# Performance work log

Measured on AMD Instinct MI355X. Metric: run time of the kernel, lower is better.

The kernel has to match this reference:

```python
import jax, jax.numpy as jnp
import numpy as np


def setup_inputs() -> dict:
    key = jax.random.key(0)
    k1, k2 = jax.random.split(key)
    B, C, D = 131072, 1024, 512
    x = jax.random.normal(k1, (B, D), dtype=jnp.float32)
    centers = jax.random.normal(k2, (C, D), dtype=jnp.float32)
    return {"x": x, "centers": centers}


def reference(x, centers):
    x_sq = jnp.sum(x * x, axis=1, keepdims=True)            # [B, 1]
    c_sq = jnp.sum(centers * centers, axis=1)               # [C]
    cross = jnp.einsum('bd,cd->bc', x, centers)             # [B, C]
    distances = jnp.maximum(x_sq + c_sq[None, :] - 2.0 * cross, 0.0)
    # softmin over clusters = softmax(-distances)
    prob = jax.nn.softmax(-distances, axis=1)
    return (distances, prob)
```

## Files before the change

kernel.cpp:

```cpp
#include <hip/hip_runtime.h>
#include <stdint.h>

#define NROWS 131072
#define NC 1024
#define ND 512
#define BM 32

using f32x4   = __attribute__((ext_vector_type(4))) float;
using bf16x8  = __attribute__((ext_vector_type(8))) short;
using short2v = __attribute__((ext_vector_type(2))) short;
using float2v = __attribute__((ext_vector_type(2))) float;
using float4v = __attribute__((ext_vector_type(4))) float;

__device__ __forceinline__ uint16_t f32_bf16(float f) {
  uint32_t u = __builtin_bit_cast(uint32_t, f);
  u += 0x7FFFu + ((u >> 16) & 1u);
  return (uint16_t)(u >> 16);
}
__device__ __forceinline__ float bf16_f32(uint16_t h) {
  uint32_t u = ((uint32_t)h) << 16;
  return __builtin_bit_cast(float, u);
}

__device__ __forceinline__ void gload_lds16(const void* g, void* l) {
  __builtin_amdgcn_global_load_lds(
      (const __attribute__((address_space(1))) unsigned int*)g,
      (__attribute__((address_space(3))) unsigned int*)l, 16, 0, 0);
}

__global__ __launch_bounds__(64) void prep_centers(
    const float* __restrict__ centers,
    uint16_t* __restrict__ cs_hi, uint16_t* __restrict__ cs_lo,
    float* __restrict__ csq) {
  const int c = blockIdx.x;
  const int t = threadIdx.x;
  const float* row = centers + (size_t)c * ND;
  const int k0 = t * 8;
  float v[8];
#pragma unroll
  for (int i = 0; i < 8; ++i) v[i] = row[k0 + i];
  float ss = 0.f;
#pragma unroll
  for (int i = 0; i < 8; ++i) ss += v[i] * v[i];
#pragma unroll
  for (int m = 1; m < 64; m <<= 1) ss += __shfl_xor(ss, m);
  if (t == 0) csq[c] = ss;

  const int kk = t >> 2;
  const int j  = t & 3;
  const int p  = j ^ (c & 3);
  const size_t off = (size_t)kk * 32768 + (size_t)c * 32 + (size_t)p * 8;
#pragma unroll
  for (int i = 0; i < 8; ++i) {
    uint16_t h = f32_bf16(v[i]);
    uint16_t l = f32_bf16(v[i] - bf16_f32(h));
    cs_hi[off + i] = h;
    cs_lo[off + i] = l;
  }
}

__global__ __launch_bounds__(512)
__attribute__((amdgpu_waves_per_eu(4)))
void kmeans_fused(
    const float* __restrict__ x,
    const uint16_t* __restrict__ cs_hi, const uint16_t* __restrict__ cs_lo,
    const float* __restrict__ csq,
    float* __restrict__ dist, float* __restrict__ prob) {
  __shared__ __align__(16) char bs[65536];
  __shared__ __align__(16) char as_hi[2048];
  __shared__ __align__(16) char as_lo[2048];
  __shared__ float xsq[BM];

  const int tid  = threadIdx.x;
  const int lane = tid & 63;
  const int wid  = tid >> 6;
  const int row0 = blockIdx.x * BM;
  const int ar = tid >> 4;
  const int ac = tid & 15;

  auto stage = [&](const uint16_t* base, int kk) {
    const char* srcb = (const char*)(base + (size_t)kk * 32768);
#pragma unroll
    for (int i = 0; i < 8; ++i) {
      const int o = (tid + i * 512) * 16;
      gload_lds16(srcb + o, bs + o);
    }
  };
  auto xload = [&](int kk) -> float2v {
    return *(const float2v*)(x + (size_t)(row0 + ar) * ND + kk * 32 + ac * 2);
  };
  auto awrite = [&](float2v v) {
    const int p = (ac >> 2) ^ (ar & 3);
    const int off = ar * 64 + p * 16 + (ac & 3) * 4;
    short2v h, l;
#pragma unroll
    for (int i = 0; i < 2; ++i) {
      uint16_t hb = f32_bf16(v[i]);
      h[i] = (short)hb;
      l[i] = (short)f32_bf16(v[i] - bf16_f32(hb));
    }
    *(short2v*)(as_hi + off) = h;
    *(short2v*)(as_lo + off) = l;
  };

  f32x4 acc[2][8];
  const f32x4 z = {0.f, 0.f, 0.f, 0.f};
#pragma unroll
  for (int mr = 0; mr < 2; ++mr)
#pragma unroll
    for (int n = 0; n < 8; ++n) acc[mr][n] = z;

  const int swz  = (((lane >> 4) ^ (lane & 3)) << 4);
  const int aoff = (lane & 15) * 64 + swz;
  const int boff = (wid * 128 + (lane & 15)) * 64 + swz;

  float xacc = 0.f;

#pragma unroll 1
  for (int s = 0; s < 16; ++s) {
    stage(cs_hi, s);
    float2v v = xload(s);
    awrite(v);
    xacc += v[0] * v[0] + v[1] * v[1];
    __syncthreads();
    {
      bf16x8 ah0 = *(const bf16x8*)(as_hi + aoff);
      bf16x8 ah1 = *(const bf16x8*)(as_hi + aoff + 1024);
      bf16x8 al0 = *(const bf16x8*)(as_lo + aoff);
      bf16x8 al1 = *(const bf16x8*)(as_lo + aoff + 1024);
#pragma unroll
      for (int n = 0; n < 8; ++n) {
        bf16x8 b = *(const bf16x8*)(bs + boff + n * 1024);
        acc[0][n] = __builtin_amdgcn_mfma_f32_16x16x32_bf16(ah0, b, acc[0][n], 0, 0, 0);
        acc[1][n] = __builtin_amdgcn_mfma_f32_16x16x32_bf16(ah1, b, acc[1][n], 0, 0, 0);
        acc[0][n] = __builtin_amdgcn_mfma_f32_16x16x32_bf16(al0, b, acc[0][n], 0, 0, 0);
        acc[1][n] = __builtin_amdgcn_mfma_f32_16x16x32_bf16(al1, b, acc[1][n], 0, 0, 0);
      }
    }
    __syncthreads();
  }

#pragma unroll 1
  for (int s = 0; s < 16; ++s) {
    stage(cs_lo, s);
    float2v v = xload(s);
    awrite(v);
    __syncthreads();
    {
      bf16x8 ah0 = *(const bf16x8*)(as_hi + aoff);
      bf16x8 ah1 = *(const bf16x8*)(as_hi + aoff + 1024);
#pragma unroll
      for (int n = 0; n < 8; ++n) {
        bf16x8 b = *(const bf16x8*)(bs + boff + n * 1024);
        acc[0][n] = __builtin_amdgcn_mfma_f32_16x16x32_bf16(ah0, b, acc[0][n], 0, 0, 0);
        acc[1][n] = __builtin_amdgcn_mfma_f32_16x16x32_bf16(ah1, b, acc[1][n], 0, 0, 0);
      }
    }
    __syncthreads();
  }

  xacc += __shfl_xor(xacc, 1);
  xacc += __shfl_xor(xacc, 2);
  xacc += __shfl_xor(xacc, 4);
  xacc += __shfl_xor(xacc, 8);
  if (ac == 0) xsq[ar] = xacc;

  float* ldsT = (float*)bs;
  const int rsub = (lane >> 4) * 4;
#pragma unroll
  for (int p = 0; p < 2; ++p) {
#pragma unroll
    for (int n = 0; n < 8; ++n)
#pragma unroll
      for (int r = 0; r < 4; ++r) {
        const int lrow = rsub + r;
        const int col = wid * 128 + n * 16 + (lane & 15);
        ldsT[lrow * 1024 + (col ^ (((lrow >> 2) & 3) << 3))] = acc[p][n][r];
      }
    __syncthreads();
#pragma unroll
    for (int q = 0; q < 2; ++q) {
      const int lr = wid * 2 + q;
      const size_t grow = (size_t)(row0 + p * 16 + lr);
      const int cmask = ((lr >> 2) & 3) << 3;
      const float xq = xsq[p * 16 + lr];
      float4v dd[4];
      float dmin = 1e30f;
#pragma unroll
      for (int j = 0; j < 4; ++j) {
        const int f = lane * 4 + j * 256;
        float4v raw = *(const float4v*)&ldsT[lr * 1024 + (f ^ cmask)];
        float4v cq = *(const float4v*)(csq + f);
#pragma unroll
        for (int i = 0; i < 4; ++i) {
          float d = fmaxf(xq + cq[i] - 2.0f * raw[i], 0.0f);
          dd[j][i] = d;
          dmin = fminf(dmin, d);
        }
      }
#pragma unroll
      for (int m = 1; m < 64; m <<= 1) dmin = fminf(dmin, __shfl_xor(dmin, m));
#pragma unroll
      for (int j = 0; j < 4; ++j)
        *(float4v*)(dist + grow * NC + lane * 4 + j * 256) = dd[j];
      float ssum = 0.f;
#pragma unroll
      for (int j = 0; j < 4; ++j)
#pragma unroll
        for (int i = 0; i < 4; ++i) {
          float e = __expf(dmin - dd[j][i]);
          dd[j][i] = e;
          ssum += e;
        }
#pragma unroll
      for (int m = 1; m < 64; m <<= 1) ssum += __shfl_xor(ssum, m);
      const float sinv = 1.0f / ssum;
#pragma unroll
      for (int j = 0; j < 4; ++j) {
        float4v pv;
#pragma unroll
        for (int i = 0; i < 4; ++i) pv[i] = dd[j][i] * sinv;
        *(float4v*)(prob + grow * NC + lane * 4 + j * 256) = pv;
      }
    }
    __syncthreads();
  }
}

extern "C" void kernel_launch(void* const* d_in, const int* in_sizes, int n_in,
                              void* d_out, int out_size, void* d_ws, size_t ws_size,
                              hipStream_t stream) {
  const float* x = (const float*)d_in[0];
  const float* centers = (const float*)d_in[1];
  float* dist = (float*)d_out;
  float* prob = dist + (size_t)NROWS * NC;

  uint16_t* cs_hi = (uint16_t*)d_ws;
  uint16_t* cs_lo = cs_hi + (size_t)NC * ND;
  float* csq = (float*)(cs_lo + (size_t)NC * ND);

  prep_centers<<<dim3(NC), dim3(64), 0, stream>>>(centers, cs_hi, cs_lo, csq);
  kmeans_fused<<<dim3(NROWS / BM), dim3(512), 0, stream>>>(x, cs_hi, cs_lo, csq,
                                                           dist, prob);
}
```

Baseline: 717.6 us.

## Double-buffer LDS staging and double the row tile to 64 rows

Raises the block tile from 32 to 64 rows, so each staged center tile feeds four MFMA row groups instead of two, halving center reloads per row. The two K loops merge into one 32-step loop with double-buffered LDS for both center and x tiles, so the next tile's global loads run during the current MFMAs and one barrier per step is removed. The LDS swizzle is changed to match the new x write pattern. Occupancy drops (waves_per_eu 2, about 140KB LDS per block) and accumulator registers double, which could limit latency hiding.

```diff
diff --git a/kernel.cpp b/kernel.cpp
--- a/kernel.cpp
+++ b/kernel.cpp
@@ -4,12 +4,12 @@
 #define NROWS 131072
 #define NC 1024
 #define ND 512
-#define BM 32
+#define BM 64
+#define NSTEP 32
 
 using f32x4   = __attribute__((ext_vector_type(4))) float;
 using bf16x8  = __attribute__((ext_vector_type(8))) short;
-using short2v = __attribute__((ext_vector_type(2))) short;
-using float2v = __attribute__((ext_vector_type(2))) float;
+using short4v = __attribute__((ext_vector_type(4))) short;
 using float4v = __attribute__((ext_vector_type(4))) float;
 
 __device__ __forceinline__ uint16_t f32_bf16(float f) {
@@ -48,7 +48,7 @@
 
   const int kk = t >> 2;
   const int j  = t & 3;
-  const int p  = j ^ (c & 3);
+  const int p  = j ^ ((c >> 1) & 3);
   const size_t off = (size_t)kk * 32768 + (size_t)c * 32 + (size_t)p * 8;
 #pragma unroll
   for (int i = 0; i < 8; ++i) {
@@ -60,101 +60,118 @@
 }
 
 __global__ __launch_bounds__(512)
-__attribute__((amdgpu_waves_per_eu(4)))
+__attribute__((amdgpu_waves_per_eu(2)))
 void kmeans_fused(
     const float* __restrict__ x,
     const uint16_t* __restrict__ cs_hi, const uint16_t* __restrict__ cs_lo,
     const float* __restrict__ csq,
     float* __restrict__ dist, float* __restrict__ prob) {
-  __shared__ __align__(16) char bs[65536];
-  __shared__ __align__(16) char as_hi[2048];
-  __shared__ __align__(16) char as_lo[2048];
+  __shared__ __align__(16) char bs[2][65536];
+  __shared__ __align__(16) char as_hi[2][4096];
+  __shared__ __align__(16) char as_lo[2][4096];
   __shared__ float xsq[BM];
 
   const int tid  = threadIdx.x;
   const int lane = tid & 63;
   const int wid  = tid >> 6;
   const int row0 = blockIdx.x * BM;
-  const int ar = tid >> 4;
-  const int ac = tid & 15;
-
-  auto stage = [&](const uint16_t* base, int kk) {
-    const char* srcb = (const char*)(base + (size_t)kk * 32768);
+  const int ar = tid >> 3;
+  const int ac = tid & 7;
+
+  auto stage = [&](int s) {
+    const uint16_t* base = (s < 16) ? cs_hi : cs_lo;
+    const char* srcb = (const char*)(base + (size_t)(s & 15) * 32768);
+    char* dst = bs[s & 1];
 #pragma unroll
     for (int i = 0; i < 8; ++i) {
       const int o = (tid + i * 512) * 16;
-      gload_lds16(srcb + o, bs + o);
-    }
-  };
-  auto xload = [&](int kk) -> float2v {
-    return *(const float2v*)(x + (size_t)(row0 + ar) * ND + kk * 32 + ac * 2);
-  };
-  auto awrite = [&](float2v v) {
-    const int p = (ac >> 2) ^ (ar & 3);
-    const int off = ar * 64 + p * 16 + (ac & 3) * 4;
-    short2v h, l;
-#pragma unroll
-    for (int i = 0; i < 2; ++i) {
+      gload_lds16(srcb + o, dst + o);
+    }
+  };
+  auto xload = [&](int s) -> float4v {
+    return *(const float4v*)(x + (size_t)(row0 + ar) * ND + (s & 15) * 32 + ac * 4);
+  };
+  auto awrite = [&](int s, float4v v) {
+    const int j = ac >> 1;
+    const int p = j ^ ((ar >> 1) & 3);
+    const int off = ar * 64 + p * 16 + (ac & 1) * 8;
+    short4v h, l;
+#pragma unroll
+    for (int i = 0; i < 4; ++i) {
       uint16_t hb = f32_bf16(v[i]);
       h[i] = (short)hb;
       l[i] = (short)f32_bf16(v[i] - bf16_f32(hb));
     }
-    *(short2v*)(as_hi + off) = h;
-    *(short2v*)(as_lo + off) = l;
-  };
-
-  f32x4 acc[2][8];
+    *(short4v*)(as_hi[s & 1] + off) = h;
+    *(short4v*)(as_lo[s & 1] + off) = l;
+  };
+
+  f32x4 acc[4][8];
   const f32x4 z = {0.f, 0.f, 0.f, 0.f};
 #pragma unroll
-  for (int mr = 0; mr < 2; ++mr)
+  for (int mr = 0; mr < 4; ++mr)
 #pragma unroll
     for (int n = 0; n < 8; ++n) acc[mr][n] = z;
 
-  const int swz  = (((lane >> 4) ^ (lane & 3)) << 4);
+  const int swz  = (((lane >> 4) ^ (((lane & 15) >> 1) & 3)) << 4);
   const int aoff = (lane & 15) * 64 + swz;
   const int boff = (wid * 128 + (lane & 15)) * 64 + swz;
 
+  auto compute = [&](int s) {
+    const char* bp  = bs[s & 1];
+    const char* ahp = as_hi[s & 1];
+    bf16x8 ah[4];
+#pragma unroll
+    for (int mr = 0; mr < 4; ++mr)
+      ah[mr] = *(const bf16x8*)(ahp + aoff + mr * 1024);
+    if (s < 16) {
+      const char* alp = as_lo[s & 1];
+      bf16x8 al[4];
+#pragma unroll
+      for (int mr = 0; mr < 4; ++mr)
+        al[mr] = *(const bf16x8*)(alp + aoff + mr * 1024);
+#pragma unroll
+      for (int n = 0; n < 8; ++n) {
+        bf16x8 b = *(const bf16x8*)(bp + boff + n * 1024);
+#pragma unroll
+        for (int mr = 0; mr < 4; ++mr)
+          acc[mr][n] = __builtin_amdgcn_mfma_f32_16x16x32_bf16(ah[mr], b, acc[mr][n], 0, 0, 0);
+#pragma unroll
+        for (int mr = 0; mr < 4; ++mr)
+          acc[mr][n] = __builtin_amdgcn_mfma_f32_16x16x32_bf16(al[mr], b, acc[mr][n], 0, 0, 0);
+      }
+    } else {
+#pragma unroll
+      for (int n = 0; n < 8; ++n) {
+        bf16x8 b = *(const bf16x8*)(bp + boff + n * 1024);
+#pragma unroll
+        for (int mr = 0; mr < 4; ++mr)
+          acc[mr][n] = __builtin_amdgcn_mfma_f32_16x16x32_bf16(ah[mr], b, acc[mr][n], 0, 0, 0);
+      }
+    }
+  };
+
   float xacc = 0.f;
 
+  stage(0);
+  {
+    float4v v0 = xload(0);
+    xacc += v0[0] * v0[0] + v0[1] * v0[1] + v0[2] * v0[2] + v0[3] * v0[3];
+    awrite(0, v0);
+  }
+  __syncthreads();
+
 #pragma unroll 1
-  for (int s = 0; s < 16; ++s) {
-    stage(cs_hi, s);
-    float2v v = xload(s);
-    awrite(v);
-    xacc += v[0] * v[0] + v[1] * v[1];
-    __syncthreads();
-    {
-      bf16x8 ah0 = *(const bf16x8*)(as_hi + aoff);
-      bf16x8 ah1 = *(const bf16x8*)(as_hi + aoff + 1024);
-      bf16x8 al0 = *(const bf16x8*)(as_lo + aoff);
-      bf16x8 al1 = *(const bf16x8*)(as_lo + aoff + 1024);
-#pragma unroll
-      for (int n = 0; n < 8; ++n) {
-        bf16x8 b = *(const bf16x8*)(bs + boff + n * 1024);
-        acc[0][n] = __builtin_amdgcn_mfma_f32_16x16x32_bf16(ah0, b, acc[0][n], 0, 0, 0);
-        acc[1][n] = __builtin_amdgcn_mfma_f32_16x16x32_bf16(ah1, b, acc[1][n], 0, 0, 0);
-        acc[0][n] = __builtin_amdgcn_mfma_f32_16x16x32_bf16(al0, b, acc[0][n], 0, 0, 0);
-        acc[1][n] = __builtin_amdgcn_mfma_f32_16x16x32_bf16(al1, b, acc[1][n], 0, 0, 0);
-      }
-    }
-    __syncthreads();
-  }
-
-#pragma unroll 1
-  for (int s = 0; s < 16; ++s) {
-    stage(cs_lo, s);
-    float2v v = xload(s);
-    awrite(v);
-    __syncthreads();
-    {
-      bf16x8 ah0 = *(const bf16x8*)(as_hi + aoff);
-      bf16x8 ah1 = *(const bf16x8*)(as_hi + aoff + 1024);
-#pragma unroll
-      for (int n = 0; n < 8; ++n) {
-        bf16x8 b = *(const bf16x8*)(bs + boff + n * 1024);
-        acc[0][n] = __builtin_amdgcn_mfma_f32_16x16x32_bf16(ah0, b, acc[0][n], 0, 0, 0);
-        acc[1][n] = __builtin_amdgcn_mfma_f32_16x16x32_bf16(ah1, b, acc[1][n], 0, 0, 0);
-      }
+  for (int s = 0; s < NSTEP; ++s) {
+    if (s + 1 < NSTEP) {
+      float4v vn = xload(s + 1);
+      stage(s + 1);
+      if (s + 1 < 16)
+        xacc += vn[0] * vn[0] + vn[1] * vn[1] + vn[2] * vn[2] + vn[3] * vn[3];
+      compute(s);
+      awrite(s + 1, vn);
+    } else {
+      compute(s);
     }
     __syncthreads();
   }
@@ -162,13 +179,12 @@
   xacc += __shfl_xor(xacc, 1);
   xacc += __shfl_xor(xacc, 2);
   xacc += __shfl_xor(xacc, 4);
-  xacc += __shfl_xor(xacc, 8);
   if (ac == 0) xsq[ar] = xacc;
 
   float* ldsT = (float*)bs;
   const int rsub = (lane >> 4) * 4;
 #pragma unroll
-  for (int p = 0; p < 2; ++p) {
+  for (int p = 0; p < 4; ++p) {
 #pragma unroll
     for (int n = 0; n < 8; ++n)
 #pragma unroll
```

Result: slower. 2.137 ms (+197.9%).

## Double-buffer center tiles and load x fragments directly into registers

Applied to the files above, without the earlier changes.

Replaces the single LDS buffer for center tiles with a double buffer, prefetching the next step's tile and x values while the current step computes. Manual vmcnt waits and raw barriers replace __syncthreads. Each wave now loads its own x fragment straight into registers and converts it to bf16 hi/lo, which removes the LDS staging of A and its per-step barrier. It also changes the B swizzle pattern, raises MFMA priority, and drops the waves_per_eu hint. In exchange it uses 128KB of LDS (limiting occupancy to one block per CU) and has every wave redundantly load and convert x.

```diff
diff --git a/kernel.cpp b/kernel.cpp
--- a/kernel.cpp
+++ b/kernel.cpp
@@ -5,12 +5,14 @@
 #define NC 1024
 #define ND 512
 #define BM 32
+#define NSTEP 32
 
 using f32x4   = __attribute__((ext_vector_type(4))) float;
 using bf16x8  = __attribute__((ext_vector_type(8))) short;
-using short2v = __attribute__((ext_vector_type(2))) short;
-using float2v = __attribute__((ext_vector_type(2))) float;
 using float4v = __attribute__((ext_vector_type(4))) float;
+
+#define WAITV12() asm volatile("s_waitcnt vmcnt(12)" ::: "memory")
+#define WAITV0()  asm volatile("s_waitcnt vmcnt(0)" ::: "memory")
 
 __device__ __forceinline__ uint16_t f32_bf16(float f) {
   uint32_t u = __builtin_bit_cast(uint32_t, f);
@@ -48,7 +50,7 @@
 
   const int kk = t >> 2;
   const int j  = t & 3;
-  const int p  = j ^ (c & 3);
+  const int p  = j ^ ((c >> 1) & 3);
   const size_t off = (size_t)kk * 32768 + (size_t)c * 32 + (size_t)p * 8;
 #pragma unroll
   for (int i = 0; i < 8; ++i) {
@@ -59,48 +61,32 @@
   }
 }
 
-__global__ __launch_bounds__(512)
-__attribute__((amdgpu_waves_per_eu(4)))
-void kmeans_fused(
+__global__ __launch_bounds__(512) void kmeans_fused(
     const float* __restrict__ x,
     const uint16_t* __restrict__ cs_hi, const uint16_t* __restrict__ cs_lo,
     const float* __restrict__ csq,
     float* __restrict__ dist, float* __restrict__ prob) {
-  __shared__ __align__(16) char bs[65536];
-  __shared__ __align__(16) char as_hi[2048];
-  __shared__ __align__(16) char as_lo[2048];
+  __shared__ __align__(16) char bs[2][65536];
   __shared__ float xsq[BM];
 
   const int tid  = threadIdx.x;
   const int lane = tid & 63;
   const int wid  = tid >> 6;
   const int row0 = blockIdx.x * BM;
-  const int ar = tid >> 4;
-  const int ac = tid & 15;
-
-  auto stage = [&](const uint16_t* base, int kk) {
-    const char* srcb = (const char*)(base + (size_t)kk * 32768);
-#pragma unroll
-    for (int i = 0; i < 8; ++i) {
-      const int o = (tid + i * 512) * 16;
-      gload_lds16(srcb + o, bs + o);
-    }
-  };
-  auto xload = [&](int kk) -> float2v {
-    return *(const float2v*)(x + (size_t)(row0 + ar) * ND + kk * 32 + ac * 2);
-  };
-  auto awrite = [&](float2v v) {
-    const int p = (ac >> 2) ^ (ar & 3);
-    const int off = ar * 64 + p * 16 + (ac & 3) * 4;
-    short2v h, l;
-#pragma unroll
-    for (int i = 0; i < 2; ++i) {
-      uint16_t hb = f32_bf16(v[i]);
-      h[i] = (short)hb;
-      l[i] = (short)f32_bf16(v[i] - bf16_f32(hb));
-    }
-    *(short2v*)(as_hi + off) = h;
-    *(short2v*)(as_lo + off) = l;
+  const int arow = lane & 15;
+  const int kq   = lane >> 4;
+
+  const float* xa0 = x + (size_t)(row0 + arow) * ND + kq * 8;
+  const float* xa1 = xa0 + (size_t)16 * ND;
+
+  auto stage = [&](int s) {
+    const uint16_t* base = (s < 16) ? cs_hi : cs_lo;
+    const char* srcb = (const char*)(base + (size_t)(s & 15) * 32768);
+    char* dst = bs[s & 1];
+    const int o = tid * 16;
+#pragma unroll
+    for (int i = 0; i < 8; ++i)
+      gload_lds16(srcb + o + i * 8192, dst + o + i * 8192);
   };
 
   f32x4 acc[2][8];
@@ -110,60 +96,110 @@
 #pragma unroll
     for (int n = 0; n < 8; ++n) acc[mr][n] = z;
 
-  const int swz  = (((lane >> 4) ^ (lane & 3)) << 4);
-  const int aoff = (lane & 15) * 64 + swz;
-  const int boff = (wid * 128 + (lane & 15)) * 64 + swz;
-
-  float xacc = 0.f;
-
-#pragma unroll 1
-  for (int s = 0; s < 16; ++s) {
-    stage(cs_hi, s);
-    float2v v = xload(s);
-    awrite(v);
-    xacc += v[0] * v[0] + v[1] * v[1];
-    __syncthreads();
-    {
-      bf16x8 ah0 = *(const bf16x8*)(as_hi + aoff);
-      bf16x8 ah1 = *(const bf16x8*)(as_hi + aoff + 1024);
-      bf16x8 al0 = *(const bf16x8*)(as_lo + aoff);
-      bf16x8 al1 = *(const bf16x8*)(as_lo + aoff + 1024);
+  const int swz  = ((kq ^ ((arow >> 1) & 3)) << 4);
+  const int boff = (wid * 128 + arow) * 64 + swz;
+
+  float xacc0 = 0.f, xacc1 = 0.f;
+
+  bf16x8 ah0, ah1, al0, al1;
+  auto cvt = [&](int s, const float4v& a0a, const float4v& a0b,
+                 const float4v& a1a, const float4v& a1b) {
+    float v0[8] = {a0a[0], a0a[1], a0a[2], a0a[3], a0b[0], a0b[1], a0b[2], a0b[3]};
+    float v1[8] = {a1a[0], a1a[1], a1a[2], a1a[3], a1b[0], a1b[1], a1b[2], a1b[3]};
+#pragma unroll
+    for (int i = 0; i < 8; ++i) {
+      uint16_t h0 = f32_bf16(v0[i]);
+      uint16_t h1 = f32_bf16(v1[i]);
+      ah0[i] = (short)h0;
+      ah1[i] = (short)h1;
+    }
+    if (s < 16) {
+#pragma unroll
+      for (int i = 0; i < 8; ++i) {
+        al0[i] = (short)f32_bf16(v0[i] - bf16_f32((uint16_t)(unsigned short)ah0[i]));
+        al1[i] = (short)f32_bf16(v1[i] - bf16_f32((uint16_t)(unsigned short)ah1[i]));
+        xacc0 += v0[i] * v0[i];
+        xacc1 += v1[i] * v1[i];
+      }
+    }
+  };
+
+  auto compute = [&](int s) {
+    const char* bp = bs[s & 1];
+    __builtin_amdgcn_s_setprio(1);
+    if (s < 16) {
 #pragma unroll
       for (int n = 0; n < 8; ++n) {
-        bf16x8 b = *(const bf16x8*)(bs + boff + n * 1024);
+        bf16x8 b = *(const bf16x8*)(bp + boff + n * 1024);
         acc[0][n] = __builtin_amdgcn_mfma_f32_16x16x32_bf16(ah0, b, acc[0][n], 0, 0, 0);
         acc[1][n] = __builtin_amdgcn_mfma_f32_16x16x32_bf16(ah1, b, acc[1][n], 0, 0, 0);
         acc[0][n] = __builtin_amdgcn_mfma_f32_16x16x32_bf16(al0, b, acc[0][n], 0, 0, 0);
         acc[1][n] = __builtin_amdgcn_mfma_f32_16x16x32_bf16(al1, b, acc[1][n], 0, 0, 0);
       }
-    }
-    __syncthreads();
-  }
-
-#pragma unroll 1
-  for (int s = 0; s < 16; ++s) {
-    stage(cs_lo, s);
-    float2v v = xload(s);
-    awrite(v);
-    __syncthreads();
-    {
-      bf16x8 ah0 = *(const bf16x8*)(as_hi + aoff);
-      bf16x8 ah1 = *(const bf16x8*)(as_hi + aoff + 1024);
+    } else {
 #pragma unroll
       for (int n = 0; n < 8; ++n) {
-        bf16x8 b = *(const bf16x8*)(bs + boff + n * 1024);
+        bf16x8 b = *(const bf16x8*)(bp + boff + n * 1024);
         acc[0][n] = __builtin_amdgcn_mfma_f32_16x16x32_bf16(ah0, b, acc[0][n], 0, 0, 0);
         acc[1][n] = __builtin_amdgcn_mfma_f32_16x16x32_bf16(ah1, b, acc[1][n], 0, 0, 0);
       }
     }
-    __syncthreads();
-  }
-
-  xacc += __shfl_xor(xacc, 1);
-  xacc += __shfl_xor(xacc, 2);
-  xacc += __shfl_xor(xacc, 4);
-  xacc += __shfl_xor(xacc, 8);
-  if (ac == 0) xsq[ar] = xacc;
+    __builtin_amdgcn_s_setprio(0);
+  };
+
+  float4v Ax0a, Ax0b, Ax1a, Ax1b;
+  float4v Ay0a, Ay0b, Ay1a, Ay1b;
+  stage(0);
+  {
+    const float* p0 = xa0;
+    const float* p1 = xa1;
+    Ax0a = *(const float4v*)p0;       Ax0b = *(const float4v*)(p0 + 4);
+    Ax1a = *(const float4v*)p1;       Ax1b = *(const float4v*)(p1 + 4);
+  }
+
+#pragma unroll 1
+  for (int s2 = 0; s2 < NSTEP; s2 += 2) {
+    {
+      const int sn = s2 + 1;
+      stage(sn);
+      const float* p0 = xa0 + (sn & 15) * 32;
+      const float* p1 = xa1 + (sn & 15) * 32;
+      Ay0a = *(const float4v*)p0;     Ay0b = *(const float4v*)(p0 + 4);
+      Ay1a = *(const float4v*)p1;     Ay1b = *(const float4v*)(p1 + 4);
+      WAITV12();
+      cvt(s2, Ax0a, Ax0b, Ax1a, Ax1b);
+      __builtin_amdgcn_s_barrier();
+      compute(s2);
+      __builtin_amdgcn_s_barrier();
+    }
+    {
+      const int s = s2 + 1;
+      const int sn = s2 + 2;
+      if (sn < NSTEP) {
+        stage(sn);
+        const float* p0 = xa0 + (sn & 15) * 32;
+        const float* p1 = xa1 + (sn & 15) * 32;
+        Ax0a = *(const float4v*)p0;   Ax0b = *(const float4v*)(p0 + 4);
+        Ax1a = *(const float4v*)p1;   Ax1b = *(const float4v*)(p1 + 4);
+        WAITV12();
+      } else {
+        WAITV0();
+      }
+      cvt(s, Ay0a, Ay0b, Ay1a, Ay1b);
+      __builtin_amdgcn_s_barrier();
+      compute(s);
+      __builtin_amdgcn_s_barrier();
+    }
+  }
+
+  xacc0 += __shfl_xor(xacc0, 16);
+  xacc0 += __shfl_xor(xacc0, 32);
+  xacc1 += __shfl_xor(xacc1, 16);
+  xacc1 += __shfl_xor(xacc1, 32);
+  if (wid == 0 && lane < 16) {
+    xsq[arow] = xacc0;
+    xsq[arow + 16] = xacc1;
+  }
 
   float* ldsT = (float*)bs;
   const int rsub = (lane >> 4) * 4;
@@ -174,7 +210,7 @@
 #pragma unroll
       for (int r = 0; r < 4; ++r) {
         const int lrow = rsub + r;
-        const int col = wid * 128 + n * 16 + (lane & 15);
+        const int col = wid * 128 + n * 16 + arow;
         ldsT[lrow * 1024 + (col ^ (((lrow >> 2) & 3) << 3))] = acc[p][n][r];
       }
     __syncthreads();
```

Result: slower. 1.158 ms (+61.3%).
